# Performance work log

Hardware: AMD Instinct MI355X
Metric: run time of the kernel (lower is better)

Reference implementation:

```python
import jax, jax.numpy as jnp
import numpy as np

B, N, C, H = 8, 2048, 256, 4
RES = 2048
OUT_C = 1


def _split_heads(t, h):
    b, n, hd = t.shape
    return t.reshape(b, n, h, hd // h).transpose(0, 2, 1, 3)


def _merge_heads(t):
    b, h, n, d = t.shape
    return t.transpose(0, 2, 1, 3).reshape(b, n, h * d)


def _inst_norm(x, eps=1e-5):
    # torch InstanceNorm1d applied per-token over head dim, no affine, biased var
    mu = jnp.mean(x, -1, keepdims=True)
    var = jnp.mean((x - mu) ** 2, -1, keepdims=True)
    return (x - mu) / jnp.sqrt(var + eps)


def _layer_norm(x, g, b, eps=1e-5):
    mu = jnp.mean(x, -1, keepdims=True)
    var = jnp.mean((x - mu) ** 2, -1, keepdims=True)
    return (x - mu) / jnp.sqrt(var + eps) * g + b


def _rot_half(x):
    d = x.shape[-1] // 2
    return jnp.concatenate([-x[..., d:], x[..., :d]], axis=-1)


def _rotary_freqs(coords, dim, mult):
    # RotaryEmbedding: t * (scale/min_freq), outer with inv_freq, cat(f, f)
    inv = 1.0 / (10000.0 ** (jnp.arange(0, dim, 2, dtype=jnp.float32) / dim))
    f = (coords * mult)[..., None] * inv  # [..., dim//2]
    return jnp.concatenate([f, f], axis=-1)


def _apply_rot(t, f):
    return t * jnp.cos(f) + _rot_half(t) * jnp.sin(f)


def _gelu(x):
    return jax.nn.gelu(x, approximate=False)


def setup_inputs():
    key = jax.random.key(0)
    ks = jax.random.split(key, 20)
    def rn(k, shp, s=0.02):
        return jax.random.normal(k, shp, dtype=jnp.float32) * s
    return {
        "z": jax.random.normal(ks[0], (B, N, C), jnp.float32),
        "propagate_pos": jax.random.uniform(ks[1], (B, N, 1), jnp.float32),
        # Gaussian Fourier feature matrix (fixed, scale=8)
        "B_fourier": jax.random.normal(ks[2], (1, C), jnp.float32) * 8.0,
        "W_coord": rn(ks[3], (2 * C, C)),
        # CrossLinearAttention (heads=4, dim_head=C, project_query=False)
        "W_kv": rn(ks[4], (C, 2 * H * C)),
        "Wo_ca": rn(ks[5], (H * C, C)),
        "bo_ca": jnp.zeros((C,), jnp.float32),
        # CrossFormer FFN (mlp_dim=C)
        "Wf1": rn(ks[6], (C, C)), "bf1": jnp.zeros((C,), jnp.float32),
        "Wf2": rn(ks[7], (C, C)), "bf2": jnp.zeros((C,), jnp.float32),
        # propagator: LayerNorm + 3-layer GELU MLP (no biases)
        "ln_g": jnp.ones((C,), jnp.float32), "ln_b": jnp.zeros((C,), jnp.float32),
        "P1": rn(ks[8], (C + 1, C)), "P2": rn(ks[9], (C, C)), "P3": rn(ks[10], (C, C)),
        # decode LinearAttention (heads=1, dim_head=C)
        "W_qkv": rn(ks[11], (C, 3 * C)),
        "Wo_da": rn(ks[12], (C, C)), "bo_da": jnp.zeros((C,), jnp.float32),
        # decode FFN
        "ln2_g": jnp.ones((C,), jnp.float32), "ln2_b": jnp.zeros((C,), jnp.float32),
        "D1": rn(ks[13], (C, C)), "D2": rn(ks[14], (C, C // 2)),
        "D3": rn(ks[15], (C // 2, OUT_C)), "b3": jnp.zeros((OUT_C,), jnp.float32),
    }


def reference(z, propagate_pos, B_fourier, W_coord, W_kv, Wo_ca, bo_ca,
              Wf1, bf1, Wf2, bf2, ln_g, ln_b, P1, P2, P3,
              W_qkv, Wo_da, bo_da, ln2_g, ln2_b, D1, D2, D3, b3):
    pos = propagate_pos  # [B, N, 1]
    n = z.shape[1]
    # --- coordinate projection: Gaussian Fourier features -> GELU -> Linear ---
    xp = 2.0 * np.pi * ((pos / 16.0) @ B_fourier)            # [B, N, C]
    feat = jnp.concatenate([jnp.sin(xp), jnp.cos(xp)], -1)   # [B, N, 2C]
    x = _gelu(feat) @ W_coord                                # [B, N, C]
    # --- cross linear attention ('fourier', heads=4, dim_head=C, q unprojected) ---
    k, v = jnp.split(z @ W_kv, 2, axis=-1)
    k = _split_heads(k, H)
    v = _split_heads(v, H)                                   # [B, H, N, C]
    q = jnp.broadcast_to(x[:, None], (x.shape[0], H, n, C))  # repeat query over heads
    q = _inst_norm(q)
    k = _inst_norm(k)
    f = _rotary_freqs(pos[..., 0], C, float(RES))[:, None]   # scale/min_freq = res
    q = _apply_rot(q, f)
    k = _apply_rot(k, f)                                     # z_pos=None -> same freqs
    dots = jnp.einsum('bhnd,bhne->bhde', k, v)               # [B, H, C, C]
    out = jnp.einsum('bhnd,bhde->bhne', q, dots) / n
    x = _merge_heads(out) @ Wo_ca + bo_ca + x
    # --- CrossFormer FFN + residual ---
    x = _gelu(x @ Wf1 + bf1) @ Wf2 + bf2 + x
    # --- propagator: LN, concat(pos/16), 3-layer GELU MLP, residual ---
    h = jnp.concatenate([_layer_norm(x, ln_g, ln_b), pos / 16.0], -1)
    zp = _gelu(_gelu(h @ P1) @ P2) @ P3 + x
    # --- decode: linear self-attention (heads=1, fourier) + FFN ---
    q2, k2, v2 = jnp.split(zp @ W_qkv, 3, axis=-1)           # each [B, N, C]
    q2 = _inst_norm(q2)
    k2 = _inst_norm(k2)
    f2 = _rotary_freqs(pos[..., 0], C, float(RES))
    q2 = _apply_rot(q2, f2)
    k2 = _apply_rot(k2, f2)
    dots2 = jnp.einsum('bnd,bne->bde', k2, v2)               # [B, C, C]
    att = jnp.einsum('bnd,bde->bne', q2, dots2) / n
    zd = att @ Wo_da + bo_da + zp
    h2 = _layer_norm(zd, ln2_g, ln2_b)
    u = _gelu(_gelu(h2 @ D1) @ D2) @ D3 + b3                 # [B, N, OUT_C]
    u = jnp.transpose(u, (0, 2, 1))                          # 'b n (t c) -> b (t c) n', t=1
    return (u, zp)
```

## Files before the change

kernel.cpp:

```cpp
#include <hip/hip_runtime.h>
#include <hip/hip_bf16.h>

using bf16 = __hip_bfloat16;
typedef __attribute__((ext_vector_type(8))) short short8;
typedef __attribute__((ext_vector_type(4))) short short4v;
typedef __attribute__((ext_vector_type(4))) float f32x4;

constexpr int BB = 8;
constexpr int NN = 2048;
constexpr int CC = 256;
constexpr int NTOK = BB * NN;
constexpr float TWO_PI = 6.283185307179586f;
constexpr float LOG2_1E4 = 13.287712379549449f;

__device__ __forceinline__ float gelu_f(float x) {
  return 0.5f * x * (1.0f + erff(x * 0.7071067811865475f));
}
__device__ __forceinline__ float us2f(unsigned short u) {
  return __uint_as_float(((unsigned)u) << 16);
}
__device__ __forceinline__ int xcd_swz(int f, int nwg) {
  return (f & 7) * (nwg >> 3) + (f >> 3);
}

// ... 8 lines not shown
#pragma unroll
    for (int o = 32; o; o >>= 1) { s += __shfl_down(s, o); s2 += __shfl_down(s2, o); }
    if (l == 0) {
      float m = s * (1.f / 256.f);
      float var = fmaxf(s2 * (1.f / 256.f) - m * m, 0.f);
      mu[w] = m; rs[w] = rsqrtf(var + eps);
    }
  }
  __syncthreads();
}

#define GLD16(src, dst)                                                       \
  __builtin_amdgcn_global_load_lds(                                           \
      (const __attribute__((address_space(1))) void*)(src),                   \
      (__attribute__((address_space(3))) void*)(dst), 16, 0, 0)

template <int K, int MI, int NB>
__device__ __forceinline__ void gemm_core(
    const bf16* __restrict__ Ap, int lda, const bf16* __restrict__ Bp,
    bf16 (&As)[NB][MI * 32 * 64], bf16 (&Bs)[NB][64 * 64], f32x4 (&acc)[MI][2]) {
  const int tid = threadIdx.x;
  const int w = tid >> 6, l = tid & 63;
  const int srow = l >> 3;
  const int scol = ((l & 7) ^ srow) * 8;
  const int rsw = (l & 7) * 8;
  const int wm = w >> 1, wn = w & 1;

  auto stage_tile = [&](int buf, int kt) {
#pragma unroll
    for (int i = 0; i < MI; ++i) {
      int r = (w * MI + i) * 8 + srow;
      GLD16(Ap + (long)r * lda + kt + scol, &As[buf][(w * MI + i) * 512 + l * 8]);
    }
#pragma unroll
    for (int i = 0; i < 2; ++i) {
      int r = (w * 2 + i) * 8 + srow;
      GLD16(Bp + (long)r * K + kt + scol, &Bs[buf][(w * 2 + i) * 512 + l * 8]);
    }
  };
  auto compute = [&](int buf) {
    short8 bfr[2][2];
#pragma unroll
    for (int ni = 0; ni < 2; ++ni)
#pragma unroll
      for (int ks = 0; ks < 2; ++ks)
        bfr[ni][ks] = *(const short8*)&Bs[buf][(wn * 32 + ni * 16 + (l & 15)) * 64 +
                                               ((ks * 32 + (l >> 4) * 8) ^ rsw)];
#pragma unroll
    for (int mi = 0; mi < MI; ++mi) {
#pragma unroll
      for (int ks = 0; ks < 2; ++ks) {
        short8 afr = *(const short8*)&As[buf][(wm * (MI * 16) + mi * 16 + (l & 15)) * 64 +
                                              ((ks * 32 + (l >> 4) * 8) ^ rsw)];
#pragma unroll
        for (int ni = 0; ni < 2; ++ni)
          acc[mi][ni] = __builtin_amdgcn_mfma_f32_16x16x32_bf16(afr, bfr[ni][ks], acc[mi][ni], 0, 0, 0);
      }
    }
  };

  if constexpr (NB == 2) {
    stage_tile(0, 0);
    asm volatile("s_waitcnt vmcnt(0)" ::: "memory");
    __builtin_amdgcn_s_barrier();
    int cur = 0;
    for (int kt = 0; kt < K; kt += 64) {
      const bool more = (kt + 64 < K);
      if (more) stage_tile(cur ^ 1, kt + 64);
      compute(cur);
      if (more) asm volatile("s_waitcnt vmcnt(0)" ::: "memory");
      __builtin_amdgcn_s_barrier();
      cur ^= 1;
    }
  } else {
    for (int kt = 0; kt < K; kt += 64) {
      stage_tile(0, kt);
      __syncthreads();
      compute(0);
      __syncthreads();
    }
  }
}

enum { E_BF16 = 0, E_BIAS_RESB_BOTH, E_BIAS_GELU, E_BIAS_RES_F32,
       E_RANK1_GELU, E_GELU, E_RES_BOTH };

template <int K, int EPI>
__global__ void __launch_bounds__(256) k_gemm(
    const bf16* __restrict__ A, int lda, const bf16* __restrict__ Bt,
    long bstride, long zstride, int nOffZ,
    const float* __restrict__ bias, const float* __restrict__ res,
    const bf16* __restrict__ resB, const float* __restrict__ rank1,
    const float* __restrict__ pvec,
    float* __restrict__ outF, bf16* __restrict__ outB, int ldo) {
  __shared__ bf16 As[1][128 * 64];
  __shared__ bf16 Bs[1][64 * 64];
  const int tid = threadIdx.x;
  const int w = tid >> 6, l = tid & 63;
  const int m0 = blockIdx.y * 128, n0 = blockIdx.x * 64;
  const int bidx = m0 >> 11;
  const bf16* Bp = Bt + (long)bidx * bstride + (long)blockIdx.z * zstride + (long)n0 * K;
  f32x4 acc[4][2] = {};
  gemm_core<K, 4, 1>(A + (long)m0 * lda, lda, Bp, As, Bs, acc);
  const int wm = w >> 1, wn = w & 1;
  const int zoff = blockIdx.z * nOffZ;
#pragma unroll
  for (int mi = 0; mi < 4; ++mi) {
#pragma unroll
    for (int ni = 0; ni < 2; ++ni) {
      const int bcol = n0 + wn * 32 + ni * 16 + (l & 15);
      const int ocol = bcol + zoff;
#pragma unroll
      for (int r = 0; r < 4; ++r) {
        const int row = m0 + wm * 64 + mi * 16 + (l >> 4) * 4 + r;
        float v = acc[mi][ni][r];
        const long oidx = (long)row * ldo + ocol;
        if constexpr (EPI == E_BF16) { outB[oidx] = __float2bfloat16(v); }
        else if constexpr (EPI == E_BIAS_RESB_BOTH) {
          v += bias[bcol] + __bfloat162float(resB[oidx]);
          outF[oidx] = v; outB[oidx] = __float2bfloat16(v);
        } else if constexpr (EPI == E_BIAS_GELU) {
          v = gelu_f(v + bias[bcol]); outB[oidx] = __float2bfloat16(v);
        } else if constexpr (EPI == E_BIAS_RES_F32) {
          v += bias[bcol] + res[oidx]; outF[oidx] = v;
        } else if constexpr (EPI == E_RANK1_GELU) {
          v = gelu_f(v + pvec[row] * rank1[bcol]); outB[oidx] = __float2bfloat16(v);
        } else if constexpr (EPI == E_GELU) {
          v = gelu_f(v); outB[oidx] = __float2bfloat16(v);
        } else {
          v += res[oidx]; outF[oidx] = v; outB[oidx] = __float2bfloat16(v);
        }
      }
    }
  }
}

template <int K>
__global__ void __launch_bounds__(256) k_gemmT(
    const bf16* __restrict__ A, int lda, const bf16* __restrict__ Bt, int nx,
    bf16* __restrict__ T0, bf16* __restrict__ T1, int thresh, int matsPerB) {
  __shared__ union {
    struct { bf16 A[1][128 * 64]; bf16 B[1][64 * 64]; } ab;
    bf16 stage[64 * 132];
  } sm;
  const int tid = threadIdx.x;
  const int w = tid >> 6, l = tid & 63;
  const int f = xcd_swz(blockIdx.x, gridDim.x);
  const int n0 = (f % nx) * 64;
  const int m0 = (f / nx) * 128;
  f32x4 acc[4][2] = {};
  gemm_core<K, 4, 1>(A + (long)m0 * lda, lda, Bt + (long)n0 * K, sm.ab.A, sm.ab.B, acc);
  const int wm = w >> 1, wn = w & 1;
  __syncthreads();
#pragma unroll
  for (int mi = 0; mi < 4; ++mi)
#pragma unroll
    for (int ni = 0; ni < 2; ++ni) {
      int c = wn * 32 + ni * 16 + (l & 15);
      int row0 = wm * 64 + mi * 16 + (l >> 4) * 4;
#pragma unroll
      for (int q = 0; q < 2; ++q) {
        bf16 b0 = __float2bfloat16(acc[mi][ni][2 * q]);
        bf16 b1 = __float2bfloat16(acc[mi][ni][2 * q + 1]);
        unsigned u = (unsigned)*(unsigned short*)&b0 |
                     ((unsigned)*(unsigned short*)&b1 << 16);
        *(unsigned*)&sm.stage[c * 132 + row0 + 2 * q] = u;
      }
    }
  __syncthreads();
  const int b = m0 >> 11, nbase = m0 & 2047;
  const int part = (n0 >= thresh) ? 1 : 0;
  const int cT0 = n0 - (part ? thresh : 0);
  bf16* dst = (part ? T1 : T0) + ((long)(b * matsPerB + (cT0 >> 8))) * 524288
            + (long)(cT0 & 255) * 2048;
  const int c = tid >> 2, ns = tid & 3;
  bf16* rowp = dst + (long)c * 2048 + nbase + ns * 8;
#pragma unroll
  for (int j = 0; j < 4; ++j) {
    short4v lo = *(const short4v*)&sm.stage[c * 132 + ns * 8 + j * 32];
    short4v hi = *(const short4v*)&sm.stage[c * 132 + ns * 8 + j * 32 + 4];
    short8 v;
    v[0] = lo[0]; v[1] = lo[1]; v[2] = lo[2]; v[3] = lo[3];
    v[4] = hi[0]; v[5] = hi[1]; v[6] = hi[2]; v[7] = hi[3];
    *(short8*)&rowp[j * 32] = v;
  }
}

__global__ void __launch_bounds__(256) k_atb2(
    const bf16* __restrict__ A0, const bf16* __restrict__ B0,
    bf16* __restrict__ D0, float scale) {
  __shared__ bf16 As[2][2 * 32 * 64];
  __shared__ bf16 Bs[2][64 * 64];
  const int tid = threadIdx.x;
  const int w = tid >> 6, l = tid & 63;
  const int f = xcd_swz(blockIdx.x, gridDim.x);
  const int n0 = (f & 3) * 64;
  const int m0 = ((f >> 2) & 3) * 64;
  const int mat = f >> 4;
  const bf16* Ap = A0 + (long)mat * 524288 + (long)m0 * 2048;
  const bf16* Bp = B0 + (long)mat * 524288 + (long)n0 * 2048;
  f32x4 acc[2][2] = {};
  gemm_core<2048, 2, 2>(Ap, 2048, Bp, As, Bs, acc);
  bf16* D = D0 + (long)mat * 65536;
  const int wm = w >> 1, wn = w & 1;
#pragma unroll
  for (int mi = 0; mi < 2; ++mi)
#pragma unroll
    for (int ni = 0; ni < 2; ++ni) {
      int col = n0 + wn * 32 + ni * 16 + (l & 15);
#pragma unroll
      for (int r = 0; r < 4; ++r) {
        int row = m0 + wm * 32 + mi * 16 + (l >> 4) * 4 + r;
        D[(long)row * 256 + col] = __float2bfloat16(acc[mi][ni][r] * scale);
      }
    }
}

__global__ void __launch_bounds__(256) k_normrot(
    bf16* __restrict__ Kt, const bf16* __restrict__ csT, int hshift) {
  __shared__ bf16 tile[256][68];
  __shared__ float ps[4][64], ps2[4][64];
  __shared__ float smu[64], srs[64];
  const int mat = blockIdx.y;
  const int tok0 = blockIdx.x * 64;
  const int b = mat >> hshift;
  const int tid = threadIdx.x;
  bf16* base = Kt + (long)mat * 524288 + tok0;
  const int cr = tid >> 3;
  const int cj = (tid & 7) * 8;
#pragma unroll
  for (int g = 0; g < 8; ++g) {
    int c = g * 32 + cr;
    *(short8*)&tile[c][cj] = *(const short8*)&base[(long)c * 2048 + cj];
  }
  __syncthreads();
  {
    const int tk = tid & 63, q = tid >> 6;
    float s = 0.f, s2 = 0.f;
#pragma unroll 8
    for (int cc = 0; cc < 64; ++cc) {
      float v = us2f(*(const unsigned short*)&tile[q * 64 + cc][tk]);
      s += v; s2 += v * v;
    }
    ps[q][tk] = s; ps2[q][tk] = s2;
  }
  __syncthreads();
  if (tid < 64) {
    float s = ps[0][tid] + ps[1][tid] + ps[2][tid] + ps[3][tid];
    float s2 = ps2[0][tid] + ps2[1][tid] + ps2[2][tid] + ps2[3][tid];
    float m = s * (1.f / 256.f);
    smu[tid] = m;
    srs[tid] = rsqrtf(fmaxf(s2 * (1.f / 256.f) - m * m, 0.f) + 1e-5f);
  }
  __syncthreads();
  const long ctok = (long)b * 2048 + tok0 + cj;
#pragma unroll
  for (int g = 0; g < 4; ++g) {
    int c = g * 32 + cr;
    short8 v0 = *(const short8*)&tile[c][cj];
    short8 v1 = *(const short8*)&tile[c + 128][cj];
    const bf16* cop = csT + (long)(c * 2) * 16384 + ctok;
    short8 co8 = *(const short8*)cop;
    short8 si8 = *(const short8*)(cop + 16384);
    short8 o0, o1;
#pragma unroll
    for (int e = 0; e < 8; ++e) {
      float m = smu[cj + e], r = srs[cj + e];
      float a = (us2f((unsigned short)v0[e]) - m) * r;
      float bb = (us2f((unsigned short)v1[e]) - m) * r;
      float co = us2f((unsigned short)co8[e]);
      float si = us2f((unsigned short)si8[e]);
      bf16 t0 = __float2bfloat16(a * co - bb * si);
      bf16 t1 = __float2bfloat16(bb * co + a * si);
      o0[e] = *(short*)&t0; o1[e] = *(short*)&t1;
    }
    *(short8*)&base[(long)c * 2048 + cj] = o0;
    *(short8*)&base[(long)(c + 128) * 2048 + cj] = o1;
  }
}

__global__ void __launch_bounds__(256) k_rotq(
    const bf16* __restrict__ in, bf16* __restrict__ out, const bf16* __restrict__ cs) {
  __shared__ float xr[4][CC];
  __shared__ float mu[4], rs[4];
  int tid = threadIdx.x;
  long tok0 = (long)blockIdx.x * 4;
#pragma unroll
  for (int t = 0; t < 4; ++t) xr[t][tid] = __bfloat162float(in[(tok0 + t) * 256 + tid]);
  stats_rows<4>(xr, mu, rs, 1e-5f);
  int i = tid & 127;
#pragma unroll
  for (int t = 0; t < 4; ++t) {
    float co = __bfloat162float(cs[(tok0 + t) * 256 + i]);
    float si = __bfloat162float(cs[(tok0 + t) * 256 + 128 + i]);
    float n0 = (xr[t][tid] - mu[t]) * rs[t];
    float n1 = (xr[t][tid ^ 128] - mu[t]) * rs[t];
    float o = (tid < 128) ? (n0 * co - n1 * si) : (n0 * co + n1 * si);
    out[(tok0 + t) * 256 + tid] = __float2bfloat16(o);
  }
}

struct WEnt { const float* s; bf16* d; int K; int N; int blk0; };
struct WTab { WEnt e[12]; };

__global__ void __launch_bounds__(256) k_wprep(WTab t) {
  int bid = blockIdx.x;
  int ei = 0;
#pragma unroll
  for (int i = 1; i < 12; ++i)
    if (bid >= t.e[i].blk0) ei = i;
  WEnt e = t.e[ei];
  int local = (bid - e.blk0) * 256 + threadIdx.x;
  if (local < e.K * e.N) {
    int n = local / e.K, k = local - n * e.K;
    e.d[local] = __float2bfloat16(e.s[(long)k * e.N + n]);
  }
}

__global__ void __launch_bounds__(256) k_csT(
    const float* __restrict__ pos, bf16* __restrict__ csT) {
  const int c = blockIdx.y;
  const int n = blockIdx.x * 256 + threadIdx.x;
  float inv = exp2f(-((float)c * (1.f / 128.f)) * LOG2_1E4);
  float fh = pos[n] * 2048.f * inv;
  float s, co; sincosf(fh, &s, &co);
  csT[(long)(c * 2) * 16384 + n] = __float2bfloat16(co);
  csT[(long)(c * 2 + 1) * 16384 + n] = __float2bfloat16(s);
}

__global__ void __launch_bounds__(256) k_pre(
    const float* __restrict__ pos, const float* __restrict__ Bf,
    const float* __restrict__ z, const float* __restrict__ P1,
    bf16* __restrict__ gf, bf16* __restrict__ cs,
    float* __restrict__ pvec, bf16* __restrict__ zb, float* __restrict__ P1L) {
  int tid = threadIdx.x;
  long tok0 = (long)blockIdx.x * 4;
  if (blockIdx.x == 0) P1L[tid] = P1[65536 + tid];
  float p[4];
#pragma unroll
  for (int t = 0; t < 4; ++t) p[t] = pos[tok0 + t];
  if (tid < 4) pvec[tok0 + tid] = p[tid] * 0.0625f;
  float bfc = Bf[tid];
#pragma unroll
  for (int t = 0; t < 4; ++t) {
    float xp = TWO_PI * (p[t] * 0.0625f) * bfc;
    float s, c; sincosf(xp, &s, &c);
    gf[(tok0 + t) * 512 + tid] = __float2bfloat16(gelu_f(s));
    gf[(tok0 + t) * 512 + 256 + tid] = __float2bfloat16(gelu_f(c));
    zb[(tok0 + t) * 256 + tid] = __float2bfloat16(z[(tok0 + t) * 256 + tid]);
  }
  if (tid < 128) {
    float inv = exp2f(-((float)tid * (1.f / 128.f)) * LOG2_1E4);
#pragma unroll
    for (int t = 0; t < 4; ++t) {
      float fh = p[t] * 2048.f * inv;
      float s, c; sincosf(fh, &s, &c);
      cs[(tok0 + t) * 256 + tid] = __float2bfloat16(c);
      cs[(tok0 + t) * 256 + 128 + tid] = __float2bfloat16(s);
    }
  }
}

__global__ void __launch_bounds__(256) k_ln(
    const float* __restrict__ xin, const float* __restrict__ g,
    const float* __restrict__ b, bf16* __restrict__ hout) {
  __shared__ float xr[4][CC];
  __shared__ float mu[4], rs[4];
  int tid = threadIdx.x;
  long tok0 = (long)blockIdx.x * 4;
#pragma unroll
  for (int t = 0; t < 4; ++t) xr[t][tid] = xin[(tok0 + t) * 256 + tid];
  stats_rows<4>(xr, mu, rs, 1e-5f);
  float gv = g[tid], bv = b[tid];
#pragma unroll
  for (int t = 0; t < 4; ++t)
    hout[(tok0 + t) * 256 + tid] = __float2bfloat16((xr[t][tid] - mu[t]) * rs[t] * gv + bv);
}

__global__ void __launch_bounds__(256) k_final(
    const bf16* __restrict__ g2, const float* __restrict__ D3,
    const float* __restrict__ b3, float* __restrict__ u) {
  int w = threadIdx.x >> 6, l = threadIdx.x & 63;
  long tok = (long)blockIdx.x * 4 + w;
  float s = __bfloat162float(g2[tok * 128 + l]) * D3[l]
          + __bfloat162float(g2[tok * 128 + 64 + l]) * D3[64 + l];
#pragma unroll
  for (int o = 32; o; o >>= 1) s += __shfl_down(s, o);
  if (l == 0) u[tok] = s + b3[0];
}

extern "C" void kernel_launch(void* const* d_in, const int* in_sizes, int n_in,
                              void* d_out, int out_size, void* d_ws, size_t ws_size,
                              hipStream_t stream) {
  const float* z    = (const float*)d_in[0];
  const float* pos  = (const float*)d_in[1];
  const float* Bf   = (const float*)d_in[2];
  const float* Wc   = (const float*)d_in[3];
  const float* Wkv  = (const float*)d_in[4];
  const float* Woca = (const float*)d_in[5];
  const float* boca = (const float*)d_in[6];
  const float* Wf1  = (const float*)d_in[7];
  const float* bf1  = (const float*)d_in[8];
  const float* Wf2  = (const float*)d_in[9];
  const float* bf2  = (const float*)d_in[10];
  const float* lng  = (const float*)d_in[11];
  const float* lnb  = (const float*)d_in[12];
  const float* P1   = (const float*)d_in[13];
  const float* P2   = (const float*)d_in[14];
  const float* P3   = (const float*)d_in[15];
  const float* Wqkv = (const float*)d_in[16];
  const float* Woda = (const float*)d_in[17];
  const float* boda = (const float*)d_in[18];
  const float* ln2g = (const float*)d_in[19];
  const float* ln2b = (const float*)d_in[20];
  const float* D1   = (const float*)d_in[21];
  const float* D2   = (const float*)d_in[22];
  const float* D3   = (const float*)d_in[23];
  const float* b3   = (const float*)d_in[24];

  float* u  = (float*)d_out;
  float* zp = (float*)d_out + NTOK;

  const long MB = 1048576L;
  char* ws = (char*)d_ws;
  bf16*  cs   = (bf16*)(ws);
  bf16*  csT  = (bf16*)(ws + 8 * MB);
  float* pvec = (float*)(ws + 16 * MB);
  long wo = 16 * MB + 65536;
  bf16* WcT   = (bf16*)(ws + wo);               wo += 262144;
  bf16* WkvT  = (bf16*)(ws + wo);               wo += 1048576;
  bf16* WocaT = (bf16*)(ws + wo);               wo += 524288;
  bf16* Wf1T  = (bf16*)(ws + wo);               wo += 131072;
  bf16* Wf2T  = (bf16*)(ws + wo);               wo += 131072;
  bf16* P1T   = (bf16*)(ws + wo);               wo += 131072;
  bf16* P2T   = (bf16*)(ws + wo);               wo += 131072;
  bf16* P3T   = (bf16*)(ws + wo);               wo += 131072;
  bf16* WqkvT = (bf16*)(ws + wo);               wo += 393216;
  bf16* WodaT = (bf16*)(ws + wo);               wo += 131072;
  bf16* D1T   = (bf16*)(ws + wo);               wo += 131072;
  bf16* D2T   = (bf16*)(ws + wo);               wo += 65536;
  float* P1L  = (float*)(ws + wo);              wo += 1024;
  char* AR = ws + 24 * MB;
  bf16*  xb     = (bf16*)(AR);
  bf16*  zb     = (bf16*)(AR + 8 * MB);
  bf16*  gf     = (bf16*)(AR + 48 * MB);
  bf16*  Kt     = (bf16*)(AR + 16 * MB);
  bf16*  Vt     = (bf16*)(AR + 48 * MB);
  bf16*  dotsT  = (bf16*)(AR + 8 * MB);
  bf16*  qrot   = (bf16*)(AR + 16 * MB);
  bf16*  merged = (bf16*)(AR + 24 * MB);
  float* x2     = (float*)(AR + 56 * MB);
  bf16*  x2b    = (bf16*)(AR + 72 * MB);
  bf16*  t1     = (bf16*)(AR + 8 * MB);
  float* x3     = (float*)(AR + 16 * MB);
  bf16*  h      = (bf16*)(AR + 32 * MB);
  bf16*  p1o    = (bf16*)(AR + 40 * MB);
  bf16*  p2o    = (bf16*)(AR + 48 * MB);
  bf16*  zpb    = (bf16*)(AR + 56 * MB);
  bf16*  q2b    = (bf16*)(AR + 64 * MB);
  bf16*  k2t    = (bf16*)(AR + 72 * MB);
  bf16*  v2t    = (bf16*)(AR + 8 * MB);
  bf16*  dots2T = (bf16*)(AR + 16 * MB);
  bf16*  att    = (bf16*)(AR + 24 * MB);
  float* zd     = (float*)(AR + 32 * MB);
  bf16*  h2     = (bf16*)(AR + 8 * MB);
  bf16*  g1     = (bf16*)(AR + 16 * MB);
  bf16*  g2     = (bf16*)(AR + 24 * MB);

  WTab tab;
  int nb = 0;
  auto add = [&](int i, const float* s, bf16* d, int K_, int N_) {
    tab.e[i].s = s; tab.e[i].d = d; tab.e[i].K = K_; tab.e[i].N = N_;
    tab.e[i].blk0 = nb; nb += (K_ * N_) / 256;
  };
  add(0, Wc, WcT, 512, 256);
  add(1, Wkv, WkvT, 256, 2048);
  add(2, Woca, WocaT, 1024, 256);
  add(3, Wf1, Wf1T, 256, 256);
  add(4, Wf2, Wf2T, 256, 256);
  add(5, P1, P1T, 256, 256);
  add(6, P2, P2T, 256, 256);
  add(7, P3, P3T, 256, 256);
  add(8, Wqkv, WqkvT, 256, 768);
  add(9, Woda, WodaT, 256, 256);
  add(10, D1, D1T, 256, 256);
  add(11, D2, D2T, 256, 128);
  k_wprep<<<nb, 256, 0, stream>>>(tab);

  k_pre<<<NTOK / 4, 256, 0, stream>>>(pos, Bf, z, P1, gf, cs, pvec, zb, P1L);
  k_csT<<<dim3(NTOK / 256, 128), 256, 0, stream>>>(pos, csT);
  k_gemm<512, E_BF16><<<dim3(4, 128, 1), 256, 0, stream>>>(
      gf, 512, WcT, 0, 0, 0, nullptr, nullptr, nullptr, nullptr, nullptr, nullptr, xb, 256);
  k_gemmT<256><<<32 * 128, 256, 0, stream>>>(zb, 256, WkvT, 32, Kt, Vt, 1024, 4);
  k_normrot<<<dim3(32, 32), 256, 0, stream>>>(Kt, csT, 2);
  k_atb2<<<512, 256, 0, stream>>>(Vt, Kt, dotsT, 1.f / 2048.f);
  k_rotq<<<NTOK / 4, 256, 0, stream>>>(xb, qrot, cs);
  k_gemm<256, E_BF16><<<dim3(4, 128, 4), 256, 0, stream>>>(
      qrot, 256, dotsT, 262144L, 65536L, 256, nullptr, nullptr, nullptr, nullptr, nullptr,
      nullptr, merged, 1024);
  k_gemm<1024, E_BIAS_RESB_BOTH><<<dim3(4, 128, 1), 256, 0, stream>>>(
      merged, 1024, WocaT, 0, 0, 0, boca, nullptr, xb, nullptr, nullptr, x2, x2b, 256);
  k_gemm<256, E_BIAS_GELU><<<dim3(4, 128, 1), 256, 0, stream>>>(
      x2b, 256, Wf1T, 0, 0, 0, bf1, nullptr, nullptr, nullptr, nullptr, nullptr, t1, 256);
  k_gemm<256, E_BIAS_RES_F32><<<dim3(4, 128, 1), 256, 0, stream>>>(
      t1, 256, Wf2T, 0, 0, 0, bf2, x2, nullptr, nullptr, nullptr, x3, nullptr, 256);
  k_ln<<<NTOK / 4, 256, 0, stream>>>(x3, lng, lnb, h);
  k_gemm<256, E_RANK1_GELU><<<dim3(4, 128, 1), 256, 0, stream>>>(
      h, 256, P1T, 0, 0, 0, nullptr, nullptr, nullptr, P1L, pvec, nullptr, p1o, 256);
  k_gemm<256, E_GELU><<<dim3(4, 128, 1), 256, 0, stream>>>(
      p1o, 256, P2T, 0, 0, 0, nullptr, nullptr, nullptr, nullptr, nullptr, nullptr, p2o, 256);
  k_gemm<256, E_RES_BOTH><<<dim3(4, 128, 1), 256, 0, stream>>>(
      p2o, 256, P3T, 0, 0, 0, nullptr, x3, nullptr, nullptr, nullptr, zp, zpb, 256);
  k_gemm<256, E_BF16><<<dim3(4, 128, 1), 256, 0, stream>>>(
      zpb, 256, WqkvT, 0, 0, 0, nullptr, nullptr, nullptr, nullptr, nullptr, nullptr, q2b, 256);
  k_gemmT<256><<<8 * 128, 256, 0, stream>>>(zpb, 256, WqkvT + 65536, 8, k2t, v2t, 256, 1);
  k_rotq<<<NTOK / 4, 256, 0, stream>>>(q2b, q2b, cs);
  k_normrot<<<dim3(32, 8), 256, 0, stream>>>(k2t, csT, 0);
  k_atb2<<<128, 256, 0, stream>>>(v2t, k2t, dots2T, 1.f / 2048.f);
  k_gemm<256, E_BF16><<<dim3(4, 128, 1), 256, 0, stream>>>(
      q2b, 256, dots2T, 65536L, 0, 0, nullptr, nullptr, nullptr, nullptr, nullptr,
      nullptr, att, 256);
  k_gemm<256, E_BIAS_RES_F32><<<dim3(4, 128, 1), 256, 0, stream>>>(
      att, 256, WodaT, 0, 0, 0, boda, zp, nullptr, nullptr, nullptr, zd, nullptr, 256);
  k_ln<<<NTOK / 4, 256, 0, stream>>>(zd, ln2g, ln2b, h2);
  k_gemm<256, E_GELU><<<dim3(4, 128, 1), 256, 0, stream>>>(
      h2, 256, D1T, 0, 0, 0, nullptr, nullptr, nullptr, nullptr, nullptr, nullptr, g1, 256);
  k_gemm<256, E_GELU><<<dim3(2, 128, 1), 256, 0, stream>>>(
      g1, 256, D2T, 0, 0, 0, nullptr, nullptr, nullptr, nullptr, nullptr, nullptr, g2, 128);
  k_final<<<NTOK / 4, 256, 0, stream>>>(g2, D3, b3, u);
}
```

Baseline: 398.7 us.

## Fuse FFN, propagator MLP, decoder attention and decoder MLP chains into row-block kernels

Replaces chains of separate GEMM, LayerNorm and final-reduction launches with four fused kernels. Each processes a 64-token row block and keeps the intermediate activations in LDS across consecutive GEMMs, with LayerNorm fused in as a prologue and the final dot with D3 as an epilogue. This removes many global round trips for the intermediates and about ten launches. In exchange, the grid is only 256 blocks, the LDS footprint per block is larger (up to about 72 KB), and the tile loop has no double buffering, so occupancy and latency hiding may suffer.

Result: slower. 480.1 us (+20.4%).

```diff
diff --git a/kernel.cpp b/kernel.cpp
--- a/kernel.cpp
+++ b/kernel.cpp
@@ -114,16 +114,287 @@
   }
 }
 
-enum { E_BF16 = 0, E_BIAS_RESB_BOTH, E_BIAS_GELU, E_BIAS_RES_F32,
-       E_RANK1_GELU, E_GELU, E_RES_BOTH };
+template <int R>
+__device__ __forceinline__ void stage_gB(const bf16* __restrict__ src, int ld, bf16* dst) {
+  const int tid = threadIdx.x;
+#pragma unroll
+  for (int it = 0; it < R / 32; ++it) {
+    int chunk = it * 256 + tid;
+    int row = chunk >> 3;
+    int sc = ((chunk & 7) ^ (row & 7)) * 8;
+    GLD16(src + (long)row * ld + sc, dst + chunk * 8);
+  }
+}
+
+template <int NI>
+__device__ __forceinline__ void compute_wide(
+    const bf16* __restrict__ As, const bf16* __restrict__ Bs, f32x4 (&acc)[4][NI]) {
+  const int l = threadIdx.x & 63, w = threadIdx.x >> 6;
+  const int rsw = (l & 7) * 8;
+  short8 bfr[NI][2];
+#pragma unroll
+  for (int ni = 0; ni < NI; ++ni)
+#pragma unroll
+    for (int ks = 0; ks < 2; ++ks)
+      bfr[ni][ks] = *(const short8*)&Bs[(w * (NI * 16) + ni * 16 + (l & 15)) * 64 +
+                                        ((ks * 32 + (l >> 4) * 8) ^ rsw)];
+#pragma unroll
+  for (int mi = 0; mi < 4; ++mi)
+#pragma unroll
+    for (int ks = 0; ks < 2; ++ks) {
+      short8 afr = *(const short8*)&As[(mi * 16 + (l & 15)) * 64 +
+                                       ((ks * 32 + (l >> 4) * 8) ^ rsw)];
+#pragma unroll
+      for (int ni = 0; ni < NI; ++ni)
+        acc[mi][ni] = __builtin_amdgcn_mfma_f32_16x16x32_bf16(afr, bfr[ni][ks], acc[mi][ni], 0, 0, 0);
+    }
+}
+
+template <int NI, int MODE>
+__device__ __forceinline__ void store_t(
+    f32x4 (&acc)[4][NI], const float* __restrict__ badd,
+    const float* __restrict__ pvec, int m0, bf16* tb) {
+  const int l = threadIdx.x & 63, w = threadIdx.x >> 6;
+#pragma unroll
+  for (int mi = 0; mi < 4; ++mi)
+#pragma unroll
+    for (int ni = 0; ni < NI; ++ni) {
+      int col = w * (NI * 16) + ni * 16 + (l & 15);
+      float bv = (MODE >= 2) ? badd[col] : 0.f;
+#pragma unroll
+      for (int r = 0; r < 4; ++r) {
+        int row = mi * 16 + (l >> 4) * 4 + r;
+        float v = acc[mi][ni][r];
+        if constexpr (MODE == 2) v += bv;
+        if constexpr (MODE == 3) v += pvec[m0 + row] * bv;
+        if constexpr (MODE >= 1) v = gelu_f(v);
+        bf16 o = __float2bfloat16(v);
+        tb[(col >> 6) * 4096 + row * 64 + ((col & 63) ^ ((row & 7) * 8))] = o;
+      }
+    }
+}
+
+__device__ __forceinline__ void ln_to_lds(
+    const float* __restrict__ xin, int m0, const float* __restrict__ g,
+    const float* __restrict__ b, bf16* hb) {
+  const int t = threadIdx.x;
+  const int row = t >> 2, seg = (t & 3) * 64;
+  const float* xr = xin + (long)(m0 + row) * 256 + seg;
+  float xv[64];
+  float s = 0.f, s2 = 0.f;
+#pragma unroll
+  for (int i = 0; i < 16; ++i) {
+    float4 v4 = *(const float4*)&xr[i * 4];
+    xv[i * 4] = v4.x; xv[i * 4 + 1] = v4.y; xv[i * 4 + 2] = v4.z; xv[i * 4 + 3] = v4.w;
+    s += v4.x + v4.y + v4.z + v4.w;
+    s2 += v4.x * v4.x + v4.y * v4.y + v4.z * v4.z + v4.w * v4.w;
+  }
+  s += __shfl_xor(s, 1); s2 += __shfl_xor(s2, 1);
+  s += __shfl_xor(s, 2); s2 += __shfl_xor(s2, 2);
+  float m = s * (1.f / 256.f);
+  float rsv = rsqrtf(fmaxf(s2 * (1.f / 256.f) - m * m, 0.f) + 1e-5f);
+#pragma unroll
+  for (int i = 0; i < 32; ++i) {
+    int c0 = seg + i * 2;
+    float v0 = (xv[i * 2] - m) * rsv * g[c0] + b[c0];
+    float v1 = (xv[i * 2 + 1] - m) * rsv * g[c0 + 1] + b[c0 + 1];
+    bf16 b0 = __float2bfloat16(v0), b1 = __float2bfloat16(v1);
+    unsigned u = (unsigned)*(unsigned short*)&b0 | ((unsigned)*(unsigned short*)&b1 << 16);
+    *(unsigned*)&hb[(c0 >> 6) * 4096 + row * 64 + ((c0 & 63) ^ ((row & 7) * 8))] = u;
+  }
+}
+
+__global__ void __launch_bounds__(256) k_ffn_fused(
+    const bf16* __restrict__ x2b, const float* __restrict__ x2,
+    const bf16* __restrict__ W1T, const float* __restrict__ bf1,
+    const bf16* __restrict__ W2T, const float* __restrict__ bf2,
+    float* __restrict__ x3) {
+  __shared__ bf16 As[4096];
+  __shared__ bf16 Bs[16384];
+  __shared__ bf16 tb[16384];
+  const int m0 = blockIdx.x * 64;
+  const int l = threadIdx.x & 63, w = threadIdx.x >> 6;
+  f32x4 acc[4][4] = {};
+  for (int kt = 0; kt < 256; kt += 64) {
+    stage_gB<64>(x2b + (long)m0 * 256 + kt, 256, As);
+    stage_gB<256>(W1T + kt, 256, Bs);
+    __syncthreads();
+    compute_wide<4>(As, Bs, acc);
+    __syncthreads();
+  }
+  store_t<4, 2>(acc, bf1, nullptr, 0, tb);
+  __syncthreads();
+  f32x4 acc2[4][4] = {};
+  for (int kt = 0; kt < 4; ++kt) {
+    stage_gB<256>(W2T + kt * 64, 256, Bs);
+    __syncthreads();
+    compute_wide<4>(tb + kt * 4096, Bs, acc2);
+    __syncthreads();
+  }
+#pragma unroll
+  for (int mi = 0; mi < 4; ++mi)
+#pragma unroll
+    for (int ni = 0; ni < 4; ++ni) {
+      int col = w * 64 + ni * 16 + (l & 15);
+      float bv = bf2[col];
+#pragma unroll
+      for (int r = 0; r < 4; ++r) {
+        long row = m0 + mi * 16 + (l >> 4) * 4 + r;
+        x3[row * 256 + col] = acc2[mi][ni][r] + bv + x2[row * 256 + col];
+      }
+    }
+}
+
+__global__ void __launch_bounds__(256) k_prop_fused(
+    const float* __restrict__ x3, const float* __restrict__ lng,
+    const float* __restrict__ lnb, const bf16* __restrict__ P1T,
+    const float* __restrict__ P1L, const float* __restrict__ pvec,
+    const bf16* __restrict__ P2T, const bf16* __restrict__ P3T,
+    float* __restrict__ zp, bf16* __restrict__ zpb) {
+  __shared__ bf16 Bs[16384];
+  __shared__ bf16 tb[16384];
+  const int m0 = blockIdx.x * 64;
+  const int l = threadIdx.x & 63, w = threadIdx.x >> 6;
+  ln_to_lds(x3, m0, lng, lnb, tb);
+  __syncthreads();
+  f32x4 acc[4][4] = {};
+  for (int kt = 0; kt < 4; ++kt) {
+    stage_gB<256>(P1T + kt * 64, 256, Bs);
+    __syncthreads();
+    compute_wide<4>(tb + kt * 4096, Bs, acc);
+    __syncthreads();
+  }
+  store_t<4, 3>(acc, P1L, pvec, m0, tb);
+  __syncthreads();
+  f32x4 acc2[4][4] = {};
+  for (int kt = 0; kt < 4; ++kt) {
+    stage_gB<256>(P2T + kt * 64, 256, Bs);
+    __syncthreads();
+    compute_wide<4>(tb + kt * 4096, Bs, acc2);
+    __syncthreads();
+  }
+  store_t<4, 1>(acc2, nullptr, nullptr, 0, tb);
+  __syncthreads();
+  f32x4 acc3[4][4] = {};
+  for (int kt = 0; kt < 4; ++kt) {
+    stage_gB<256>(P3T + kt * 64, 256, Bs);
+    __syncthreads();
+    compute_wide<4>(tb + kt * 4096, Bs, acc3);
+    __syncthreads();
+  }
+#pragma unroll
+  for (int mi = 0; mi < 4; ++mi)
+#pragma unroll
+    for (int ni = 0; ni < 4; ++ni) {
+      int col = w * 64 + ni * 16 + (l & 15);
+#pragma unroll
+      for (int r = 0; r < 4; ++r) {
+        long row = m0 + mi * 16 + (l >> 4) * 4 + r;
+        float v = acc3[mi][ni][r] + x3[row * 256 + col];
+        zp[row * 256 + col] = v;
+        zpb[row * 256 + col] = __float2bfloat16(v);
+      }
+    }
+}
+
+__global__ void __launch_bounds__(256) k_attdec_fused(
+    const bf16* __restrict__ q2b, const bf16* __restrict__ dots2T,
+    const bf16* __restrict__ WodaT, const float* __restrict__ boda,
+    const float* __restrict__ zp, float* __restrict__ zd) {
+  __shared__ bf16 As[4096];
+  __shared__ bf16 Bs[16384];
+  __shared__ bf16 tb[16384];
+  const int m0 = blockIdx.x * 64;
+  const int l = threadIdx.x & 63, w = threadIdx.x >> 6;
+  const bf16* Bp = dots2T + (long)(m0 >> 11) * 65536;
+  f32x4 acc[4][4] = {};
+  for (int kt = 0; kt < 256; kt += 64) {
+    stage_gB<64>(q2b + (long)m0 * 256 + kt, 256, As);
+    stage_gB<256>(Bp + kt, 256, Bs);
+    __syncthreads();
+    compute_wide<4>(As, Bs, acc);
+    __syncthreads();
+  }
+  store_t<4, 0>(acc, nullptr, nullptr, 0, tb);
+  __syncthreads();
+  f32x4 acc2[4][4] = {};
+  for (int kt = 0; kt < 4; ++kt) {
+    stage_gB<256>(WodaT + kt * 64, 256, Bs);
+    __syncthreads();
+    compute_wide<4>(tb + kt * 4096, Bs, acc2);
+    __syncthreads();
+  }
+#pragma unroll
+  for (int mi = 0; mi < 4; ++mi)
+#pragma unroll
+    for (int ni = 0; ni < 4; ++ni) {
+      int col = w * 64 + ni * 16 + (l & 15);
+      float bv = boda[col];
+#pragma unroll
+      for (int r = 0; r < 4; ++r) {
+        long row = m0 + mi * 16 + (l >> 4) * 4 + r;
+        zd[row * 256 + col] = acc2[mi][ni][r] + bv + zp[row * 256 + col];
+      }
+    }
+}
+
+__global__ void __launch_bounds__(256) k_dec_fused(
+    const float* __restrict__ zd, const float* __restrict__ ln2g,
+    const float* __restrict__ ln2b, const bf16* __restrict__ D1T,
+    const bf16* __restrict__ D2T, const float* __restrict__ D3,
+    const float* __restrict__ b3, float* __restrict__ u) {
+  __shared__ bf16 Bs[16384];
+  __shared__ bf16 tb[16384];
+  const int m0 = blockIdx.x * 64;
+  const int l = threadIdx.x & 63, w = threadIdx.x >> 6;
+  ln_to_lds(zd, m0, ln2g, ln2b, tb);
+  __syncthreads();
+  f32x4 acc[4][4] = {};
+  for (int kt = 0; kt < 4; ++kt) {
+    stage_gB<256>(D1T + kt * 64, 256, Bs);
+    __syncthreads();
+    compute_wide<4>(tb + kt * 4096, Bs, acc);
+    __syncthreads();
+  }
+  store_t<4, 1>(acc, nullptr, nullptr, 0, tb);
+  __syncthreads();
+  f32x4 acc2[4][2] = {};
+  for (int kt = 0; kt < 4; ++kt) {
+    stage_gB<128>(D2T + kt * 64, 256, Bs);
+    __syncthreads();
+    compute_wide<2>(tb + kt * 4096, Bs, acc2);
+    __syncthreads();
+  }
+#pragma unroll
+  for (int mi = 0; mi < 4; ++mi)
+#pragma unroll
+    for (int ni = 0; ni < 2; ++ni) {
+      int col = w * 32 + ni * 16 + (l & 15);
+#pragma unroll
+      for (int r = 0; r < 4; ++r) {
+        int row = mi * 16 + (l >> 4) * 4 + r;
+        Bs[row * 128 + col] = __float2bfloat16(gelu_f(acc2[mi][ni][r]));
+      }
+    }
+  __syncthreads();
+  const int t = threadIdx.x;
+  const int row = t >> 2, seg = (t & 3) * 32;
+  float s = 0.f;
+#pragma unroll
+  for (int i = 0; i < 32; ++i)
+    s += __bfloat162float(Bs[row * 128 + seg + i]) * D3[seg + i];
+  s += __shfl_xor(s, 1);
+  s += __shfl_xor(s, 2);
+  if ((t & 3) == 0) u[m0 + row] = s + b3[0];
+}
+
+enum { E_BF16 = 0, E_BIAS_RESB_BOTH };
 
 template <int K, int EPI>
 __global__ void __launch_bounds__(256) k_gemm(
     const bf16* __restrict__ A, int lda, const bf16* __restrict__ Bt,
     long bstride, long zstride, int nOffZ,
-    const float* __restrict__ bias, const float* __restrict__ res,
-    const bf16* __restrict__ resB, const float* __restrict__ rank1,
-    const float* __restrict__ pvec,
+    const float* __restrict__ bias, const bf16* __restrict__ resB,
     float* __restrict__ outF, bf16* __restrict__ outB, int ldo) {
   __shared__ bf16 As[1][128 * 64];
   __shared__ bf16 Bs[1][64 * 64];
@@ -147,20 +418,11 @@
         const int row = m0 + wm * 64 + mi * 16 + (l >> 4) * 4 + r;
         float v = acc[mi][ni][r];
         const long oidx = (long)row * ldo + ocol;
-        if constexpr (EPI == E_BF16) { outB[oidx] = __float2bfloat16(v); }
-        else if constexpr (EPI == E_BIAS_RESB_BOTH) {
+        if constexpr (EPI == E_BF16) {
+          outB[oidx] = __float2bfloat16(v);
+        } else {
           v += bias[bcol] + __bfloat162float(resB[oidx]);
           outF[oidx] = v; outB[oidx] = __float2bfloat16(v);
-        } else if constexpr (EPI == E_BIAS_GELU) {
-          v = gelu_f(v + bias[bcol]); outB[oidx] = __float2bfloat16(v);
-        } else if constexpr (EPI == E_BIAS_RES_F32) {
-          v += bias[bcol] + res[oidx]; outF[oidx] = v;
-        } else if constexpr (EPI == E_RANK1_GELU) {
-          v = gelu_f(v + pvec[row] * rank1[bcol]); outB[oidx] = __float2bfloat16(v);
-        } else if constexpr (EPI == E_GELU) {
-          v = gelu_f(v); outB[oidx] = __float2bfloat16(v);
-        } else {
-          v += res[oidx]; outF[oidx] = v; outB[oidx] = __float2bfloat16(v);
         }
       }
     }
@@ -391,34 +653,6 @@
       cs[(tok0 + t) * 256 + 128 + tid] = __float2bfloat16(s);
     }
   }
-}
-
-__global__ void __launch_bounds__(256) k_ln(
-    const float* __restrict__ xin, const float* __restrict__ g,
-    const float* __restrict__ b, bf16* __restrict__ hout) {
-  __shared__ float xr[4][CC];
-  __shared__ float mu[4], rs[4];
-  int tid = threadIdx.x;
-  long tok0 = (long)blockIdx.x * 4;
-#pragma unroll
-  for (int t = 0; t < 4; ++t) xr[t][tid] = xin[(tok0 + t) * 256 + tid];
-  stats_rows<4>(xr, mu, rs, 1e-5f);
-  float gv = g[tid], bv = b[tid];
-#pragma unroll
-  for (int t = 0; t < 4; ++t)
-    hout[(tok0 + t) * 256 + tid] = __float2bfloat16((xr[t][tid] - mu[t]) * rs[t] * gv + bv);
-}
-
-__global__ void __launch_bounds__(256) k_final(
-    const bf16* __restrict__ g2, const float* __restrict__ D3,
-    const float* __restrict__ b3, float* __restrict__ u) {
-  int w = threadIdx.x >> 6, l = threadIdx.x & 63;
-  long tok = (long)blockIdx.x * 4 + w;
-  float s = __bfloat162float(g2[tok * 128 + l]) * D3[l]
-          + __bfloat162float(g2[tok * 128 + 64 + l]) * D3[64 + l];
-#pragma unroll
-  for (int o = 32; o; o >>= 1) s += __shfl_down(s, o);
-  if (l == 0) u[tok] = s + b3[0];
 }
 
 extern "C" void kernel_launch(void* const* d_in, const int* in_sizes, int n_in,
@@ -483,21 +717,13 @@
   bf16*  merged = (bf16*)(AR + 24 * MB);
   float* x2     = (float*)(AR + 56 * MB);
   bf16*  x2b    = (bf16*)(AR + 72 * MB);
-  bf16*  t1     = (bf16*)(AR + 8 * MB);
   float* x3     = (float*)(AR + 16 * MB);
-  bf16*  h      = (bf16*)(AR + 32 * MB);
-  bf16*  p1o    = (bf16*)(AR + 40 * MB);
-  bf16*  p2o    = (bf16*)(AR + 48 * MB);
-  bf16*  zpb    = (bf16*)(AR + 56 * MB);
-  bf16*  q2b    = (bf16*)(AR + 64 * MB);
-  bf16*  k2t    = (bf16*)(AR + 72 * MB);
-  bf16*  v2t    = (bf16*)(AR + 8 * MB);
-  bf16*  dots2T = (bf16*)(AR + 16 * MB);
-  bf16*  att    = (bf16*)(AR + 24 * MB);
-  float* zd     = (float*)(AR + 32 * MB);
-  bf16*  h2     = (bf16*)(AR + 8 * MB);
-  bf16*  g1     = (bf16*)(AR + 16 * MB);
-  bf16*  g2     = (bf16*)(AR + 24 * MB);
+  bf16*  zpb    = (bf16*)(AR + 32 * MB);
+  bf16*  q2b    = (bf16*)(AR + 40 * MB);
+  bf16*  k2t    = (bf16*)(AR + 48 * MB);
+  bf16*  v2t    = (bf16*)(AR + 56 * MB);
+  bf16*  dots2T = (bf16*)(AR + 8 * MB);
+  float* zd     = (float*)(AR + 64 * MB);
 
   WTab tab;
   int nb = 0;
@@ -522,42 +748,24 @@
   k_pre<<<NTOK / 4, 256, 0, stream>>>(pos, Bf, z, P1, gf, cs, pvec, zb, P1L);
   k_csT<<<dim3(NTOK / 256, 128), 256, 0, stream>>>(pos, csT);
   k_gemm<512, E_BF16><<<dim3(4, 128, 1), 256, 0, stream>>>(
-      gf, 512, WcT, 0, 0, 0, nullptr, nullptr, nullptr, nullptr, nullptr, nullptr, xb, 256);
+      gf, 512, WcT, 0, 0, 0, nullptr, nullptr, nullptr, xb, 256);
   k_gemmT<256><<<32 * 128, 256, 0, stream>>>(zb, 256, WkvT, 32, Kt, Vt, 1024, 4);
   k_normrot<<<dim3(32, 32), 256, 0, stream>>>(Kt, csT, 2);
   k_atb2<<<512, 256, 0, stream>>>(Vt, Kt, dotsT, 1.f / 2048.f);
   k_rotq<<<NTOK / 4, 256, 0, stream>>>(xb, qrot, cs);
   k_gemm<256, E_BF16><<<dim3(4, 128, 4), 256, 0, stream>>>(
-      qrot, 256, dotsT, 262144L, 65536L, 256, nullptr, nullptr, nullptr, nullptr, nullptr,
-      nullptr, merged, 1024);
+      qrot, 256, dotsT, 262144L, 65536L, 256, nullptr, nullptr, nullptr, merged, 1024);
   k_gemm<1024, E_BIAS_RESB_BOTH><<<dim3(4, 128, 1), 256, 0, stream>>>(
-      merged, 1024, WocaT, 0, 0, 0, boca, nullptr, xb, nullptr, nullptr, x2, x2b, 256);
-  k_gemm<256, E_BIAS_GELU><<<dim3(4, 128, 1), 256, 0, stream>>>(
-      x2b, 256, Wf1T, 0, 0, 0, bf1, nullptr, nullptr, nullptr, nullptr, nullptr, t1, 256);
-  k_gemm<256, E_BIAS_RES_F32><<<dim3(4, 128, 1), 256, 0, stream>>>(
-      t1, 256, Wf2T, 0, 0, 0, bf2, x2, nullptr, nullptr, nullptr, x3, nullptr, 256);
-  k_ln<<<NTOK / 4, 256, 0, stream>>>(x3, lng, lnb, h);
-  k_gemm<256, E_RANK1_GELU><<<dim3(4, 128, 1), 256, 0, stream>>>(
-      h, 256, P1T, 0, 0, 0, nullptr, nullptr, nullptr, P1L, pvec, nullptr, p1o, 256);
-  k_gemm<256, E_GELU><<<dim3(4, 128, 1), 256, 0, stream>>>(
-      p1o, 256, P2T, 0, 0, 0, nullptr, nullptr, nullptr, nullptr, nullptr, nullptr, p2o, 256);
-  k_gemm<256, E_RES_BOTH><<<dim3(4, 128, 1), 256, 0, stream>>>(
-      p2o, 256, P3T, 0, 0, 0, nullptr, x3, nullptr, nullptr, nullptr, zp, zpb, 256);
+      merged, 1024, WocaT, 0, 0, 0, boca, xb, x2, x2b, 256);
+  k_ffn_fused<<<NTOK / 64, 256, 0, stream>>>(x2b, x2, Wf1T, bf1, Wf2T, bf2, x3);
+  k_prop_fused<<<NTOK / 64, 256, 0, stream>>>(x3, lng, lnb, P1T, P1L, pvec,
+                                              P2T, P3T, zp, zpb);
   k_gemm<256, E_BF16><<<dim3(4, 128, 1), 256, 0, stream>>>(
-      zpb, 256, WqkvT, 0, 0, 0, nullptr, nullptr, nullptr, nullptr, nullptr, nullptr, q2b, 256);
+      zpb, 256, WqkvT, 0, 0, 0, nullptr, nullptr, nullptr, q2b, 256);
   k_gemmT<256><<<8 * 128, 256, 0, stream>>>(zpb, 256, WqkvT + 65536, 8, k2t, v2t, 256, 1);
   k_rotq<<<NTOK / 4, 256, 0, stream>>>(q2b, q2b, cs);
   k_normrot<<<dim3(32, 8), 256, 0, stream>>>(k2t, csT, 0);
   k_atb2<<<128, 256, 0, stream>>>(v2t, k2t, dots2T, 1.f / 2048.f);
-  k_gemm<256, E_BF16><<<dim3(4, 128, 1), 256, 0, stream>>>(
-      q2b, 256, dots2T, 65536L, 0, 0, nullptr, nullptr, nullptr, nullptr, nullptr,
-      nullptr, att, 256);
-  k_gemm<256, E_BIAS_RES_F32><<<dim3(4, 128, 1), 256, 0, stream>>>(
-      att, 256, WodaT, 0, 0, 0, boda, zp, nullptr, nullptr, nullptr, zd, nullptr, 256);
-  k_ln<<<NTOK / 4, 256, 0, stream>>>(zd, ln2g, ln2b, h2);
-  k_gemm<256, E_GELU><<<dim3(4, 128, 1), 256, 0, stream>>>(
-      h2, 256, D1T, 0, 0, 0, nullptr, nullptr, nullptr, nullptr, nullptr, nullptr, g1, 256);
-  k_gemm<256, E_GELU><<<dim3(2, 128, 1), 256, 0, stream>>>(
-      g1, 256, D2T, 0, 0, 0, nullptr, nullptr, nullptr, nullptr, nullptr, nullptr, g2, 128);
-  k_final<<<NTOK / 4, 256, 0, stream>>>(g2, D3, b3, u);
-}
+  k_attdec_fused<<<NTOK / 64, 256, 0, stream>>>(q2b, dots2T, WodaT, boda, zp, zd);
+  k_dec_fused<<<NTOK / 64, 256, 0, stream>>>(zd, ln2g, ln2b, D1T, D2T, D3, b3, u);
+}
```

## Fold cross-attention dots into output projection before applying to queries

Applied to the files above, without the earlier changes.

Reassociates q·(dots_h)·Wo into q·(dots_h·Wo_h). The per-batch head matrices are concatenated into a 256x1024 matrix, and a small GEMM first combines them with Wo_ca. This replaces a 4-head 256-K GEMM plus a 1024-K projection GEMM over all tokens with one 256-K GEMM per token. It adds a small per-batch precompute, writes dots transposed with strided stores, and changes the bf16 rounding order.

Result: faster. 389.6 us (-2.3%).

```diff
diff --git a/kernel.cpp b/kernel.cpp
--- a/kernel.cpp
+++ b/kernel.cpp
@@ -120,7 +120,7 @@
 template <int K, int EPI>
 __global__ void __launch_bounds__(256) k_gemm(
     const bf16* __restrict__ A, int lda, const bf16* __restrict__ Bt,
-    long bstride, long zstride, int nOffZ,
+    long bstride, long zstride, int nOffZ, long ozstride,
     const float* __restrict__ bias, const float* __restrict__ res,
     const bf16* __restrict__ resB, const float* __restrict__ rank1,
     const float* __restrict__ pvec,
@@ -136,6 +136,7 @@
   gemm_core<K, 4, 1>(A + (long)m0 * lda, lda, Bp, As, Bs, acc);
   const int wm = w >> 1, wn = w & 1;
   const int zoff = blockIdx.z * nOffZ;
+  const long ozoff = (long)blockIdx.z * ozstride;
 #pragma unroll
   for (int mi = 0; mi < 4; ++mi) {
 #pragma unroll
@@ -146,7 +147,7 @@
       for (int r = 0; r < 4; ++r) {
         const int row = m0 + wm * 64 + mi * 16 + (l >> 4) * 4 + r;
         float v = acc[mi][ni][r];
-        const long oidx = (long)row * ldo + ocol;
+        const long oidx = (long)row * ldo + ocol + ozoff;
         if constexpr (EPI == E_BF16) { outB[oidx] = __float2bfloat16(v); }
         else if constexpr (EPI == E_BIAS_RESB_BOTH) {
           v += bias[bcol] + __bfloat162float(resB[oidx]);
@@ -220,7 +221,7 @@
 
 __global__ void __launch_bounds__(256) k_atb2(
     const bf16* __restrict__ A0, const bf16* __restrict__ B0,
-    bf16* __restrict__ D0, float scale) {
+    bf16* __restrict__ D0, float scale, int hconcat) {
   __shared__ bf16 As[2][2 * 32 * 64];
   __shared__ bf16 Bs[2][64 * 64];
   const int tid = threadIdx.x;
@@ -233,19 +234,35 @@
   const bf16* Bp = B0 + (long)mat * 524288 + (long)n0 * 2048;
   f32x4 acc[2][2] = {};
   gemm_core<2048, 2, 2>(Ap, 2048, Bp, As, Bs, acc);
-  bf16* D = D0 + (long)mat * 65536;
   const int wm = w >> 1, wn = w & 1;
-#pragma unroll
-  for (int mi = 0; mi < 2; ++mi)
-#pragma unroll
-    for (int ni = 0; ni < 2; ++ni) {
-      int col = n0 + wn * 32 + ni * 16 + (l & 15);
-#pragma unroll
-      for (int r = 0; r < 4; ++r) {
-        int row = m0 + wm * 32 + mi * 16 + (l >> 4) * 4 + r;
-        D[(long)row * 256 + col] = __float2bfloat16(acc[mi][ni][r] * scale);
+  if (hconcat) {
+    const int b = mat >> 2, h = mat & 3;
+    bf16* D = D0 + (long)b * 262144 + h * 256;
+#pragma unroll
+    for (int mi = 0; mi < 2; ++mi)
+#pragma unroll
+      for (int ni = 0; ni < 2; ++ni) {
+        int col = n0 + wn * 32 + ni * 16 + (l & 15);
+#pragma unroll
+        for (int r = 0; r < 4; ++r) {
+          int row = m0 + wm * 32 + mi * 16 + (l >> 4) * 4 + r;
+          D[(long)col * 1024 + row] = __float2bfloat16(acc[mi][ni][r] * scale);
+        }
       }
-    }
+  } else {
+    bf16* D = D0 + (long)mat * 65536;
+#pragma unroll
+    for (int mi = 0; mi < 2; ++mi)
+#pragma unroll
+      for (int ni = 0; ni < 2; ++ni) {
+        int col = n0 + wn * 32 + ni * 16 + (l & 15);
+#pragma unroll
+        for (int r = 0; r < 4; ++r) {
+          int row = m0 + wm * 32 + mi * 16 + (l >> 4) * 4 + r;
+          D[(long)row * 256 + col] = __float2bfloat16(acc[mi][ni][r] * scale);
+        }
+      }
+  }
 }
 
 __global__ void __launch_bounds__(256) k_normrot(
@@ -478,15 +495,15 @@
   bf16*  gf     = (bf16*)(AR + 48 * MB);
   bf16*  Kt     = (bf16*)(AR + 16 * MB);
   bf16*  Vt     = (bf16*)(AR + 48 * MB);
-  bf16*  dotsT  = (bf16*)(AR + 8 * MB);
+  bf16*  dotsH  = (bf16*)(AR + 8 * MB);
+  bf16*  MwT    = (bf16*)(AR + 12 * MB);
   bf16*  qrot   = (bf16*)(AR + 16 * MB);
-  bf16*  merged = (bf16*)(AR + 24 * MB);
   float* x2     = (float*)(AR + 56 * MB);
   bf16*  x2b    = (bf16*)(AR + 72 * MB);
-  bf16*  t1     = (bf16*)(AR + 8 * MB);
-  float* x3     = (float*)(AR + 16 * MB);
-  bf16*  h      = (bf16*)(AR + 32 * MB);
-  bf16*  p1o    = (bf16*)(AR + 40 * MB);
+  bf16*  t1     = (bf16*)(AR + 24 * MB);
+  float* x3     = (float*)(AR + 32 * MB);
+  bf16*  h      = (bf16*)(AR + 16 * MB);
+  bf16*  p1o    = (bf16*)(AR + 24 * MB);
   bf16*  p2o    = (bf16*)(AR + 48 * MB);
   bf16*  zpb    = (bf16*)(AR + 56 * MB);
   bf16*  q2b    = (bf16*)(AR + 64 * MB);
@@ -522,42 +539,53 @@
   k_pre<<<NTOK / 4, 256, 0, stream>>>(pos, Bf, z, P1, gf, cs, pvec, zb, P1L);
   k_csT<<<dim3(NTOK / 256, 128), 256, 0, stream>>>(pos, csT);
   k_gemm<512, E_BF16><<<dim3(4, 128, 1), 256, 0, stream>>>(
-      gf, 512, WcT, 0, 0, 0, nullptr, nullptr, nullptr, nullptr, nullptr, nullptr, xb, 256);
+      gf, 512, WcT, 0, 0, 0, 0, nullptr, nullptr, nullptr, nullptr, nullptr,
+      nullptr, xb, 256);
   k_gemmT<256><<<32 * 128, 256, 0, stream>>>(zb, 256, WkvT, 32, Kt, Vt, 1024, 4);
   k_normrot<<<dim3(32, 32), 256, 0, stream>>>(Kt, csT, 2);
-  k_atb2<<<512, 256, 0, stream>>>(Vt, Kt, dotsT, 1.f / 2048.f);
+  k_atb2<<<512, 256, 0, stream>>>(Vt, Kt, dotsH, 1.f / 2048.f, 1);
   k_rotq<<<NTOK / 4, 256, 0, stream>>>(xb, qrot, cs);
-  k_gemm<256, E_BF16><<<dim3(4, 128, 4), 256, 0, stream>>>(
-      qrot, 256, dotsT, 262144L, 65536L, 256, nullptr, nullptr, nullptr, nullptr, nullptr,
-      nullptr, merged, 1024);
-  k_gemm<1024, E_BIAS_RESB_BOTH><<<dim3(4, 128, 1), 256, 0, stream>>>(
-      merged, 1024, WocaT, 0, 0, 0, boca, nullptr, xb, nullptr, nullptr, x2, x2b, 256);
+  k_gemm<1024, E_BF16><<<dim3(4, 2, 8), 256, 0, stream>>>(
+      WocaT, 1024, dotsH, 0, 262144L, 0, 65536L, nullptr, nullptr, nullptr,
+      nullptr, nullptr, nullptr, MwT, 256);
+  k_gemm<256, E_BIAS_RESB_BOTH><<<dim3(4, 128, 1), 256, 0, stream>>>(
+      qrot, 256, MwT, 65536L, 0, 0, 0, boca, nullptr, xb, nullptr, nullptr,
+      x2, x2b, 256);
   k_gemm<256, E_BIAS_GELU><<<dim3(4, 128, 1), 256, 0, stream>>>(
-      x2b, 256, Wf1T, 0, 0, 0, bf1, nullptr, nullptr, nullptr, nullptr, nullptr, t1, 256);
+      x2b, 256, Wf1T, 0, 0, 0, 0, bf1, nullptr, nullptr, nullptr, nullptr,
+      nullptr, t1, 256);
   k_gemm<256, E_BIAS_RES_F32><<<dim3(4, 128, 1), 256, 0, stream>>>(
-      t1, 256, Wf2T, 0, 0, 0, bf2, x2, nullptr, nullptr, nullptr, x3, nullptr, 256);
+      t1, 256, Wf2T, 0, 0, 0, 0, bf2, x2, nullptr, nullptr, nullptr,
+      x3, nullptr, 256);
   k_ln<<<NTOK / 4, 256, 0, stream>>>(x3, lng, lnb, h);
   k_gemm<256, E_RANK1_GELU><<<dim3(4, 128, 1), 256, 0, stream>>>(
-      h, 256, P1T, 0, 0, 0, nullptr, nullptr, nullptr, P1L, pvec, nullptr, p1o, 256);
+      h, 256, P1T, 0, 0, 0, 0, nullptr, nullptr, nullptr, P1L, pvec,
+      nullptr, p1o, 256);
   k_gemm<256, E_GELU><<<dim3(4, 128, 1), 256, 0, stream>>>(
-      p1o, 256, P2T, 0, 0, 0, nullptr, nullptr, nullptr, nullptr, nullptr, nullptr, p2o, 256);
+      p1o, 256, P2T, 0, 0, 0, 0, nullptr, nullptr, nullptr, nullptr, nullptr,
+      nullptr, p2o, 256);
   k_gemm<256, E_RES_BOTH><<<dim3(4, 128, 1), 256, 0, stream>>>(
-      p2o, 256, P3T, 0, 0, 0, nullptr, x3, nullptr, nullptr, nullptr, zp, zpb, 256);
+      p2o, 256, P3T, 0, 0, 0, 0, nullptr, x3, nullptr, nullptr, nullptr,
+      zp, zpb, 256);
   k_gemm<256, E_BF16><<<dim3(4, 128, 1), 256, 0, stream>>>(
-      zpb, 256, WqkvT, 0, 0, 0, nullptr, nullptr, nullptr, nullptr, nullptr, nullptr, q2b, 256);
+      zpb, 256, WqkvT, 0, 0, 0, 0, nullptr, nullptr, nullptr, nullptr, nullptr,
+      nullptr, q2b, 256);
   k_gemmT<256><<<8 * 128, 256, 0, stream>>>(zpb, 256, WqkvT + 65536, 8, k2t, v2t, 256, 1);
   k_rotq<<<NTOK / 4, 256, 0, stream>>>(q2b, q2b, cs);
   k_normrot<<<dim3(32, 8), 256, 0, stream>>>(k2t, csT, 0);
-  k_atb2<<<128, 256, 0, stream>>>(v2t, k2t, dots2T, 1.f / 2048.f);
+  k_atb2<<<128, 256, 0, stream>>>(v2t, k2t, dots2T, 1.f / 2048.f, 0);
   k_gemm<256, E_BF16><<<dim3(4, 128, 1), 256, 0, stream>>>(
-      q2b, 256, dots2T, 65536L, 0, 0, nullptr, nullptr, nullptr, nullptr, nullptr,
-      nullptr, att, 256);
+      q2b, 256, dots2T, 65536L, 0, 0, 0, nullptr, nullptr, nullptr, nullptr,
+      nullptr, nullptr, att, 256);
   k_gemm<256, E_BIAS_RES_F32><<<dim3(4, 128, 1), 256, 0, stream>>>(
-      att, 256, WodaT, 0, 0, 0, boda, zp, nullptr, nullptr, nullptr, zd, nullptr, 256);
+      att, 256, WodaT, 0, 0, 0, 0, boda, zp, nullptr, nullptr, nullptr,
+      zd, nullptr, 256);
   k_ln<<<NTOK / 4, 256, 0, stream>>>(zd, ln2g, ln2b, h2);
   k_gemm<256, E_GELU><<<dim3(4, 128, 1), 256, 0, stream>>>(
-      h2, 256, D1T, 0, 0, 0, nullptr, nullptr, nullptr, nullptr, nullptr, nullptr, g1, 256);
+      h2, 256, D1T, 0, 0, 0, 0, nullptr, nullptr, nullptr, nullptr, nullptr,
+      nullptr, g1, 256);
   k_gemm<256, E_GELU><<<dim3(2, 128, 1), 256, 0, stream>>>(
-      g1, 256, D2T, 0, 0, 0, nullptr, nullptr, nullptr, nullptr, nullptr, nullptr, g2, 128);
+      g1, 256, D2T, 0, 0, 0, 0, nullptr, nullptr, nullptr, nullptr, nullptr,
+      nullptr, g2, 128);
   k_final<<<NTOK / 4, 256, 0, stream>>>(g2, D3, b3, u);
 }
```
